# Kernel tuning notes

Hardware: AMD Instinct MI355X
Metric: run time of the kernel (lower is better)

The kernel has to match this reference:

```python
import jax, jax.numpy as jnp
import numpy as np

B, T, D, H, L, FF, V = 32, 64, 512, 8, 4, 2048, 128
HD = D // H
TEMP = 0.1
SCALE_BASE = 16.0
NEG = -1e9


def setup_inputs() -> dict:
    key = jax.random.key(0)
    cnt = [0]
    def nk():
        cnt[0] += 1
        return jax.random.fold_in(key, cnt[0])
    def rn(shape, s=0.02):
        return jax.random.normal(nk(), shape, dtype=jnp.float32) * s
    inp = {
        "target_tensor": jax.random.randint(nk(), (B, T), 0, V),
        "mol_encoding": jax.random.normal(nk(), (B, D), dtype=jnp.float32),
        "emb": rn((V, D), 1.0),
        "sa_in_w": rn((L, 3 * D, D)), "sa_in_b": jnp.zeros((L, 3 * D), jnp.float32),
        "sa_out_w": rn((L, D, D)), "sa_out_b": jnp.zeros((L, D), jnp.float32),
        "ca_in_w": rn((L, 3 * D, D)), "ca_in_b": jnp.zeros((L, 3 * D), jnp.float32),
        "ca_out_w": rn((L, D, D)), "ca_out_b": jnp.zeros((L, D), jnp.float32),
        "ff_w1": rn((L, FF, D)), "ff_b1": jnp.zeros((L, FF), jnp.float32),
        "ff_w2": rn((L, D, FF)), "ff_b2": jnp.zeros((L, D), jnp.float32),
        "n1_g": jnp.ones((L, D), jnp.float32), "n1_b": jnp.zeros((L, D), jnp.float32),
        "n2_g": jnp.ones((L, D), jnp.float32), "n2_b": jnp.zeros((L, D), jnp.float32),
        "n3_g": jnp.ones((L, D), jnp.float32), "n3_b": jnp.zeros((L, D), jnp.float32),
        "fn_g": jnp.ones((D,), jnp.float32), "fn_b": jnp.zeros((D,), jnp.float32),
        "out_w1": rn((2 * D, D)), "out_b1": jnp.zeros((2 * D,), jnp.float32),
        "out_w2": rn((1024, 2 * D)), "out_b2": jnp.zeros((1024,), jnp.float32),
        "out_w3": rn((V, 1024)), "out_b3": jnp.zeros((V,), jnp.float32),
    }
    return inp


def _ln(x, g, b, eps=1e-5):
    mu = x.mean(-1, keepdims=True)
    var = ((x - mu) ** 2).mean(-1, keepdims=True)
    return (x - mu) * jax.lax.rsqrt(var + eps) * g + b


def _xpos(x):
    # x: [B, T, D]; XPOS rotary with scale_base=16, downscale=False
    t, d = x.shape[1], x.shape[2]
    half = d // 2
    sv = (jnp.arange(0, d, 2, dtype=jnp.float32) + 0.4 * d) / (1.4 * d)      # [half]
    pos = jnp.arange(t, dtype=jnp.float32)
    scale = sv[None, :] ** (pos / SCALE_BASE)[:, None]                       # [t, half]
    inv_freq = 1.0 / (10000.0 ** (jnp.arange(half, dtype=jnp.float32) / half))
    ang = pos[:, None] * inv_freq[None, :]                                   # [t, half]
    sin = jnp.repeat(jnp.sin(ang) * scale, 2, axis=-1)                       # duplicate_interleave
    cos = jnp.repeat(jnp.cos(ang) * scale, 2, axis=-1)
    x1, x2 = x[..., ::2], x[..., 1::2]
    rot = jnp.stack((-x2, x1), axis=-1).reshape(x.shape)                     # rotate_every_two
    return x * cos + rot * sin


def _mha(q_in, k_in, v_in, in_w, in_b, out_w, out_b, mask):
    wq, wk, wv = jnp.split(in_w, 3, axis=0)
    bq, bk, bv = jnp.split(in_b, 3, axis=0)
    Bq, Tq = q_in.shape[0], q_in.shape[1]
    q = (q_in @ wq.T + bq).reshape(Bq, Tq, H, HD)
    k = (k_in @ wk.T + bk).reshape(Bq, -1, H, HD)
    v = (v_in @ wv.T + bv).reshape(Bq, -1, H, HD)
    scores = jnp.einsum('bqhd,bkhd->bhqk', q, k) / np.float32(np.sqrt(HD))
    if mask is not None:
        scores = jnp.where(mask, NEG, scores)
    p = jax.nn.softmax(scores, axis=-1)
    o = jnp.einsum('bhqk,bkhd->bqhd', p, v).reshape(Bq, Tq, D)
    return o @ out_w.T + out_b


def reference(target_tensor, mol_encoding, emb, sa_in_w, sa_in_b, sa_out_w, sa_out_b,
              ca_in_w, ca_in_b, ca_out_w, ca_out_b, ff_w1, ff_b1, ff_w2, ff_b2,
              n1_g, n1_b, n2_g, n2_b, n3_g, n3_b, fn_g, fn_b,
              out_w1, out_b1, out_w2, out_b2, out_w3, out_b3):
    memory = mol_encoding[:, None, :]                      # [B, 1, D]
    causal = jnp.triu(jnp.ones((T, T), bool), 1)
    samp_key = jax.random.key(1)

    def logits_at(pred, t):
        x = _xpos(emb[pred])                               # [B, T, D]
        mask = causal[None, None] | (pred == 0)[:, None, None, :]
        for i in range(L):
            a = _mha(x, x, x, sa_in_w[i], sa_in_b[i], sa_out_w[i], sa_out_b[i], mask)
            x = _ln(x + a, n1_g[i], n1_b[i])
            c = _mha(x, memory, memory, ca_in_w[i], ca_in_b[i], ca_out_w[i], ca_out_b[i], None)
            x = _ln(x + c, n2_g[i], n2_b[i])
            f = jax.nn.silu(x @ ff_w1[i].T + ff_b1[i]) @ ff_w2[i].T + ff_b2[i]
            x = _ln(x + f, n3_g[i], n3_b[i])
        x = _ln(x, fn_g, fn_b)
        h = jnp.take(x, t - 1, axis=1)                     # [B, D]
        h = jax.nn.gelu(h @ out_w1.T + out_b1, approximate=False)
        h = jax.nn.gelu(h @ out_w2.T + out_b2, approximate=False)
        return h @ out_w3.T + out_b3                       # [B, V]

    def step(pred, t):
        logits = logits_at(pred, t)
        lp = jax.nn.log_softmax(logits / TEMP, axis=-1)
        u = jax.random.uniform(jax.random.fold_in(samp_key, t), lp.shape)
        g = -jnp.log(-jnp.log(u + 1e-9) + 1e-9)
        tok = jnp.argmax(lp + g, axis=-1).astype(jnp.int32)
        return pred.at[:, t].set(tok), logits

    pred0 = jnp.zeros((B, T), jnp.int32).at[:, 0].set(1)
    pred, _ = jax.lax.scan(jax.checkpoint(step), pred0, jnp.arange(1, T))
    return pred
```

## Files before the change

### kernel.cpp

```cpp
#include <hip/hip_runtime.h>
#include <stdint.h>
#include <stddef.h>

#define BB 32
#define TT 64
#define DD 512
#define HH 8
#define HDIM 64
#define LL 4
#define FFD 2048
#define VV 128

#define NBLK 256
#define NTHR 512

__host__ __device__ inline uint32_t rotl32(uint32_t v, int n){ return (v << n) | (v >> (32 - n)); }

__host__ __device__ inline void tf2x32(uint32_t k0, uint32_t k1, uint32_t x0, uint32_t x1,
                                       uint32_t* o0, uint32_t* o1){
  uint32_t ks2 = k0 ^ k1 ^ 0x1BD11BDAu;
  x0 += k0; x1 += k1;
  x0 += x1; x1 = rotl32(x1,13); x1 ^= x0;
  x0 += x1; x1 = rotl32(x1,15); x1 ^= x0;
  x0 += x1; x1 = rotl32(x1,26); x1 ^= x0;
  x0 += x1; x1 = rotl32(x1, 6); x1 ^= x0;
  x0 += k1; x1 += ks2 + 1u;
  x0 += x1; x1 = rotl32(x1,17); x1 ^= x0;
  x0 += x1; x1 = rotl32(x1,29); x1 ^= x0;
  x0 += x1; x1 = rotl32(x1,16); x1 ^= x0;
  x0 += x1; x1 = rotl32(x1,24); x1 ^= x0;
  x0 += ks2; x1 += k0 + 2u;
  x0 += x1; x1 = rotl32(x1,13); x1 ^= x0;
  x0 += x1; x1 = rotl32(x1,15); x1 ^= x0;
  x0 += x1; x1 = rotl32(x1,26); x1 ^= x0;
  x0 += x1; x1 = rotl32(x1, 6); x1 ^= x0;
  x0 += k0; x1 += k1 + 3u;
  x0 += x1; x1 = rotl32(x1,17); x1 ^= x0;
  x0 += x1; x1 = rotl32(x1,29); x1 ^= x0;
  x0 += x1; x1 = rotl32(x1,16); x1 ^= x0;
  x0 += x1; x1 = rotl32(x1,24); x1 ^= x0;
  x0 += k1; x1 += ks2 + 4u;
  x0 += x1; x1 = rotl32(x1,13); x1 ^= x0;
  x0 += x1; x1 = rotl32(x1,15); x1 ^= x0;
  x0 += x1; x1 = rotl32(x1,26); x1 ^= x0;
  x0 += x1; x1 = rotl32(x1, 6); x1 ^= x0;
  x0 += ks2; x1 += k0 + 5u;
  *o0 = x0; *o1 = x1;
}

__device__ inline float dot_f4(const float* __restrict__ a, const float* __restrict__ w, int K){
  float acc = 0.f;
  const float4* a4 = (const float4*)a;
  const float4* w4 = (const float4*)w;
  int K4 = K >> 2;
  for (int k = 0; k < K4; ++k){
    float4 av = a4[k], wv = w4[k];
    acc = fmaf(av.x, wv.x, acc);
    acc = fmaf(av.y, wv.y, acc);
    acc = fmaf(av.z, wv.z, acc);
    acc = fmaf(av.w, wv.w, acc);
  }
  return acc;
}

__device__ inline float block_ln(float v, float g, float bb, float* red){
  __syncthreads();
  float s = v;
  #pragma unroll
  for (int off = 32; off; off >>= 1) s += __shfl_xor(s, off);
  if ((threadIdx.x & 63) == 0) red[threadIdx.x >> 6] = s;
  __syncthreads();
  float mu = (red[0]+red[1]+red[2]+red[3]+red[4]+red[5]+red[6]+red[7]) * (1.0f/512.0f);
  float dv = v - mu;
  float sq = dv * dv;
  #pragma unroll
  for (int off = 32; off; off >>= 1) sq += __shfl_xor(sq, off);
  __syncthreads();
  if ((threadIdx.x & 63) == 0) red[threadIdx.x >> 6] = sq;
  __syncthreads();
  float var = (red[0]+red[1]+red[2]+red[3]+red[4]+red[5]+red[6]+red[7]) * (1.0f/512.0f);
  return dv * (1.0f / sqrtf(var + 1e-5f)) * g + bb;
}

__device__ inline float row_reduce(float v, int wid, int j, float* wred){
  #pragma unroll
  for (int off = 32; off; off >>= 1) v += __shfl_xor(v, off);
  if ((threadIdx.x & 63) == 0) wred[wid] = v;
  __syncthreads();
  float r = wred[2*j] + wred[2*j+1];
  __syncthreads();
  return r;
}

__device__ __forceinline__ void gbar(unsigned* bar, int g){
  __syncthreads();
  if (threadIdx.x == 0){
    unsigned* cnt = bar + g*64;
    unsigned* gen = bar + g*64 + 16;
    __builtin_amdgcn_fence(__ATOMIC_RELEASE, "agent");
    unsigned old = __hip_atomic_load(gen, __ATOMIC_RELAXED, __HIP_MEMORY_SCOPE_AGENT);
    if (__hip_atomic_fetch_add(cnt, 1u, __ATOMIC_RELAXED, __HIP_MEMORY_SCOPE_AGENT) == 63u){
      __hip_atomic_store(cnt, 0u, __ATOMIC_RELAXED, __HIP_MEMORY_SCOPE_AGENT);
      __hip_atomic_fetch_add(gen, 1u, __ATOMIC_RELEASE, __HIP_MEMORY_SCOPE_AGENT);
    } else {
      while (__hip_atomic_load(gen, __ATOMIC_RELAXED, __HIP_MEMORY_SCOPE_AGENT) == old)
        __builtin_amdgcn_s_sleep(1);
    }
    __builtin_amdgcn_fence(__ATOMIC_ACQUIRE, "agent");
  }
  __syncthreads();
}

__global__ void k_tables(float* __restrict__ cosb, float* __restrict__ sinb){
  int tid = blockIdx.x * blockDim.x + threadIdx.x;
  int p = tid >> 8, i = tid & 255;
  float sv = (2.0f * (float)i + 204.8f) / 716.8f;
  float scale = powf(sv, (float)p / 16.0f);
  float invf = 1.0f / powf(10000.0f, (float)i / 256.0f);
  float ang = (float)p * invf;
  cosb[tid] = cosf(ang) * scale;
  sinb[tid] = sinf(ang) * scale;
}

__global__ void k_ca1(const float* __restrict__ mol, const float* __restrict__ w,
                      const float* __restrict__ bias, float* __restrict__ tmp){
  int tid = blockIdx.x * blockDim.x + threadIdx.x;
  int l = tid >> 14; int r = tid & 16383; int b = r >> 9; int d = r & 511;
  const float* wr = w + (size_t)l*3*DD*DD + (size_t)(2*DD + d)*DD;
  tmp[tid] = bias[l*3*DD + 2*DD + d] + dot_f4(mol + (size_t)b*DD, wr, DD);
}

__global__ void k_ca2(const float* __restrict__ tmp, const float* __restrict__ w,
                      const float* __restrict__ bias, float* __restrict__ cac){
  int tid = blockIdx.x * blockDim.x + threadIdx.x;
  int l = tid >> 14; int r = tid & 16383; int b = r >> 9; int d = r & 511;
  const float* wr = w + (size_t)l*DD*DD + (size_t)d*DD;
  cac[tid] = bias[l*DD + d] + dot_f4(tmp + ((size_t)l*BB + b)*DD, wr, DD);
}

__global__ void k_binit(unsigned* __restrict__ bar, int* __restrict__ pred){
  int tid = threadIdx.x;
  bar[tid] = 0u;
  pred[tid]        = ((tid & (TT-1)) == 0) ? 1 : 0;
  pred[tid + 1024] = (((tid + 1024) & (TT-1)) == 0) ? 1 : 0;
}

__global__ void k_pack32(const float* __restrict__ in, float* __restrict__ out,
                         int N, int K, int total){
  int tid = blockIdx.x * blockDim.x + threadIdx.x;
  if (tid >= total) return;
  int S = N * K;
  int l = tid / S, r = tid - l*S;
  int k32 = r / (32*N);
  int r2 = r - k32*32*N;
  int n = r2 >> 5, ku = r2 & 31;
  out[tid] = in[(size_t)l*S + (size_t)n*K + k32*32 + ku];
}

#define CELL8(WARR, KOFF)                                                     \
  _Pragma("unroll")                                                           \
  for (int q = 0; q < 8; ++q){                                                \
    float4 w = WARR[q];                                                       \
    const int kk = (KOFF) + q*4;                                              \
    _Pragma("unroll")                                                         \
    for (int r_ = 0; r_ < 8; ++r_){                                           \
      float4 x = *(const float4*)&sxp[r_*512 + kk];                           \
      a[r_]=fmaf(w.x,x.x,a[r_]); a[r_]=fmaf(w.y,x.y,a[r_]);                   \
      a[r_]=fmaf(w.z,x.z,a[r_]); a[r_]=fmaf(w.w,x.w,a[r_]);                   \
    }                                                                         \
  }

struct KParams {
  const float *emb, *sab, *sob, *f1b, *f2b;
  const float *g1,*b1,*g2,*b2,*g3,*b3,*fg,*fb;
  const float *o1b,*o2b,*o3w,*o3b;
  const float *cosb,*sinb,*cac;
  const float *sawP,*sowP,*f1wP,*f2wP,*o1wP,*o2wP;
  float *kc,*vc,*xl,*qb,*at,*ao,*x2,*fo,*h1,*xf,*hh1,*hh2,*ps3;
  int *pred;
  unsigned *bar;
};

__global__ __launch_bounds__(NTHR) void k_persist(KParams P){
  const int bid = blockIdx.x, tid = threadIdx.x;
  const int g = bid & 3;
  const int m = bid >> 2;
  const int wid = tid >> 6, lane = tid & 63;
  __shared__ __align__(16) float smem[17472];

  for (int t = 1; t < TT; ++t){
    const int pp = t - 1;

    for (int l = 0; l < LL; ++l){
      if (m < 24){
        float* sx   = smem;
        float* part = smem + 4096;
        float* srow = smem + 8192;
        if (l == 0){
          #pragma unroll
          for (int it = 0; it < 2; ++it){
            int j = it*4 + (tid >> 7), d4 = (tid & 127) * 4;
            int rb = g*8 + j;
            int tok = P.pred[rb*TT + pp];
            #pragma unroll
            for (int e = d4; e < d4 + 4; e += 2){
              int i = e >> 1;
              float c = P.cosb[pp*256 + i], s = P.sinb[pp*256 + i];
              float e0 = P.emb[(size_t)tok*DD + e];
              float e1 = P.emb[(size_t)tok*DD + e + 1];
              sx[j*512 + e]     = fmaf(e0, c, -(e1*s));
              sx[j*512 + e + 1] = fmaf(e1, c, e0*s);
            }
          }
        } else {
          if (tid < 8){
            float aa = 0.f, bq = 0.f;
            const float* pr = P.ps3 + (size_t)(g*8 + tid)*64;
            for (int s = 0; s < 32; ++s){ aa += pr[s*2]; bq += pr[s*2+1]; }
            float mu = aa * (1.0f/512.0f);
            float var = bq * (1.0f/512.0f) - mu*mu;
            srow[tid*2]   = mu;
            srow[tid*2+1] = 1.0f / sqrtf(var + 1e-5f);
          }
          __syncthreads();
          #pragma unroll
          for (int it = 0; it < 2; ++it){
            int j = it*4 + (tid >> 7), d4 = (tid & 127) * 4;
            int rb = g*8 + j;
            float mu = srow[j*2], rs = srow[j*2+1];
            float4 xv = *(const float4*)&P.x2[(size_t)rb*DD + d4];
            float4 fv = *(const float4*)&P.fo[(size_t)rb*DD + d4];
            const float* g3r = P.g3 + (size_t)(l-1)*DD;
            const float* b3r = P.b3 + (size_t)(l-1)*DD;
            float yv[4] = {xv.x+fv.x, xv.y+fv.y, xv.z+fv.z, xv.w+fv.w};
            #pragma unroll
            for (int i = 0; i < 4; ++i)
              sx[j*512 + d4 + i] = (yv[i]-mu)*rs*g3r[d4+i] + b3r[d4+i];
          }
        }
        __syncthreads();
        if (m == 0){
          #pragma unroll
          for (int it = 0; it < 2; ++it){
            int j = it*4 + (tid >> 7), d4 = (tid & 127) * 4;
            *(float4*)&P.xl[(size_t)(g*8+j)*DD + d4] = *(float4*)&sx[j*512 + d4];
          }
        }
        const int n0 = m*64;
        const float4* wb0 = (const float4*)P.sawP + ((size_t)l*16 + wid*2)*(1536*8)
                          + (size_t)(n0 + lane)*8;
        const float4* wb1 = wb0 + 1536*8;
        float4 w0[8], w1[8];
        #pragma unroll
        for (int q = 0; q < 8; ++q) w0[q] = wb0[q];
        #pragma unroll
        for (int q = 0; q < 8; ++q) w1[q] = wb1[q];
        float a[8] = {0.f,0.f,0.f,0.f,0.f,0.f,0.f,0.f};
        const float* sxp = sx;
        const int kb = wid*64;
        CELL8(w0, kb);
        CELL8(w1, kb + 32);
        #pragma unroll
        for (int r_ = 0; r_ < 8; ++r_) part[(wid*8 + r_)*64 + lane] = a[r_];
        __syncthreads();
        {
          int jr = tid >> 6, nl = tid & 63;
          int n = n0 + nl, rb2 = g*8 + jr;
          float s = P.sab[l*1536 + n];
          #pragma unroll
          for (int w = 0; w < 8; ++w) s += part[(w*8+jr)*64 + nl];
          if (n < DD){
            P.qb[(size_t)rb2*DD + n] = s;
          } else if (n < 2*DD){
            int h = (n - DD) >> 6, hd = (n - DD) & 63;
            P.kc[((((size_t)l*BB + rb2)*HH + h)*TT + pp)*HDIM + hd] = s;
          } else {
            int h = (n - 2*DD) >> 6, hd = (n - 2*DD) & 63;
            P.vc[((((size_t)l*BB + rb2)*HH + h)*TT + pp)*HDIM + hd] = s;
          }
        }
      }
      gbar(P.bar, g);

      {
        int bl = m >> 3, h = m & 7, rb = g*8 + bl;
        float* qs = smem; float* ps = smem + 64;
        if (tid < 64) qs[tid] = P.qb[(size_t)rb*DD + h*HDIM + tid];
        __syncthreads();
        if (tid < 64){
          const float* kb = P.kc + (((size_t)l*BB + rb)*HH + h)*TT*HDIM;
          float s = -INFINITY;
          if (lane <= pp && P.pred[rb*TT + lane] != 0){
            const float* kr = kb + lane*HDIM;
            float acc = 0.f;
            #pragma unroll
            for (int k2 = 0; k2 < HDIM; ++k2) acc = fmaf(qs[k2], kr[k2], acc);
            s = acc * 0.125f;
          }
          float mx = s;
          #pragma unroll
          for (int off = 32; off; off >>= 1) mx = fmaxf(mx, __shfl_xor(mx, off));
          float e = (s == -INFINITY) ? 0.f : expf(s - mx);
          float sum = e;
          #pragma unroll
          for (int off = 32; off; off >>= 1) sum += __shfl_xor(sum, off);
          ps[lane] = e / sum;
          const float* vb = P.vc + (((size_t)l*BB + rb)*HH + h)*TT*HDIM;
          float o = 0.f;
          int jj = 0;
          for (; jj + 8 <= t; jj += 8){
            float vv[8];
            #pragma unroll
            for (int u = 0; u < 8; ++u) vv[u] = vb[(jj+u)*HDIM + lane];
            #pragma unroll
            for (int u = 0; u < 8; ++u) o = fmaf(ps[jj+u], vv[u], o);
          }
          for (; jj <= pp; ++jj) o = fmaf(ps[jj], vb[jj*HDIM + lane], o);
          P.at[(size_t)rb*DD + h*HDIM + lane] = o;
        }
      }
      gbar(P.bar, g);

      if (m < 32){
        float* ats  = smem;
        float* part = smem + 4096;
        #pragma unroll
        for (int q = 0; q < 2; ++q){
          int fi = tid + q*512;
          int j = fi >> 7, c4 = fi & 127;
          *(float4*)&ats[j*512 + c4*4] = *(const float4*)&P.at[(size_t)(g*8+j)*DD + c4*4];
        }
        __syncthreads();
        const int n0 = m*16;
        const int jb = lane >> 4, nc = lane & 15;
        const float4* wb0 = (const float4*)P.sowP + ((size_t)l*16 + wid*2)*(512*8)
                          + (size_t)(n0 + nc)*8;
        const float4* wb1 = wb0 + 512*8;
        float4 w0[8], w1[8];
        #pragma unroll
        for (int q = 0; q < 8; ++q) w0[q] = wb0[q];
        #pragma unroll
        for (int q = 0; q < 8; ++q) w1[q] = wb1[q];
        float ac0 = 0.f, ac1 = 0.f;
        const int kb = wid*64;
        #pragma unroll
        for (int q = 0; q < 8; ++q){
          float4 w = w0[q];
          float4 xa = *(const float4*)&ats[jb*512 + kb + q*4];
          float4 xb = *(const float4*)&ats[(jb+4)*512 + kb + q*4];
          ac0=fmaf(w.x,xa.x,ac0); ac0=fmaf(w.y,xa.y,ac0); ac0=fmaf(w.z,xa.z,ac0); ac0=fmaf(w.w,xa.w,ac0);
          ac1=fmaf(w.x,xb.x,ac1); ac1=fmaf(w.y,xb.y,ac1); ac1=fmaf(w.z,xb.z,ac1); ac1=fmaf(w.w,xb.w,ac1);
        }
        #pragma unroll
        for (int q = 0; q < 8; ++q){
          float4 w = w1[q];
          float4 xa = *(const float4*)&ats[jb*512 + kb + 32 + q*4];
          float4 xb = *(const float4*)&ats[(jb+4)*512 + kb + 32 + q*4];
          ac0=fmaf(w.x,xa.x,ac0); ac0=fmaf(w.y,xa.y,ac0); ac0=fmaf(w.z,xa.z,ac0); ac0=fmaf(w.w,xa.w,ac0);
          ac1=fmaf(w.x,xb.x,ac1); ac1=fmaf(w.y,xb.y,ac1); ac1=fmaf(w.z,xb.z,ac1); ac1=fmaf(w.w,xb.w,ac1);
        }
        part[wid*128 + jb*16 + nc]       = ac0;
        part[wid*128 + (jb+4)*16 + nc]   = ac1;
        __syncthreads();
        if (tid < 128){
          int jb2 = tid >> 4, nc2 = tid & 15, n = n0 + nc2;
          float s = P.sob[l*DD + n];
          #pragma unroll
          for (int w = 0; w < 8; ++w) s += part[w*128 + jb2*16 + nc2];
          P.ao[(size_t)(g*8+jb2)*DD + n] = s;
        }
      }
      gbar(P.bar, g);

      if (m < 32){
        float* sx2  = smem;
        float* part = smem + 4096;
        float* wred = smem + 8192;
        #pragma unroll
        for (int it = 0; it < 2; ++it){
          int j = tid >> 7, d4 = (tid & 127) * 4;
          int jr = it*4 + j;
          int rb = g*8 + jr;
          float4 xlv = *(const float4*)&P.xl[(size_t)rb*DD + d4];
          float4 aov = *(const float4*)&P.ao[(size_t)rb*DD + d4];
          float y[4] = {xlv.x+aov.x, xlv.y+aov.y, xlv.z+aov.z, xlv.w+aov.w};
          float s = ((y[0]+y[1])+y[2])+y[3];
          float mu = row_reduce(s, wid, j, wred) * (1.0f/512.0f);
          float dv[4], sq = 0.f;
          #pragma unroll
          for (int i = 0; i < 4; ++i){ dv[i] = y[i]-mu; sq += dv[i]*dv[i]; }
          float rs = 1.0f / sqrtf(row_reduce(sq, wid, j, wred) * (1.0f/512.0f) + 1e-5f);
          float z[4];
          #pragma unroll
          for (int i = 0; i < 4; ++i){
            int d = d4 + i;
            z[i] = dv[i]*rs*P.g1[l*DD+d] + P.b1[l*DD+d] + P.cac[((size_t)l*BB + rb)*DD + d];
          }
          float s2 = ((z[0]+z[1])+z[2])+z[3];
          float mu2 = row_reduce(s2, wid, j, wred) * (1.0f/512.0f);
          float dz[4], sq2 = 0.f;
          #pragma unroll
          for (int i = 0; i < 4; ++i){ dz[i] = z[i]-mu2; sq2 += dz[i]*dz[i]; }
          float rs2 = 1.0f / sqrtf(row_reduce(sq2, wid, j, wred) * (1.0f/512.0f) + 1e-5f);
          #pragma unroll
          for (int i = 0; i < 4; ++i){
            int d = d4 + i;
            float x2v = dz[i]*rs2*P.g2[l*DD+d] + P.b2[l*DD+d];
            sx2[jr*512 + d] = x2v;
          }
        }
        __syncthreads();
        if (m == 0){
          #pragma unroll
          for (int it = 0; it < 2; ++it){
            int jr = it*4 + (tid >> 7), d4 = (tid & 127) * 4;
            *(float4*)&P.x2[(size_t)(g*8+jr)*DD + d4] = *(float4*)&sx2[jr*512 + d4];
          }
        }
        const int n0 = m*64;
        const float4* wb0 = (const float4*)P.f1wP + ((size_t)l*16 + wid*2)*(2048*8)
                          + (size_t)(n0 + lane)*8;
        const float4* wb1 = wb0 + 2048*8;
        float4 w0[8], w1[8];
        #pragma unroll
        for (int q = 0; q < 8; ++q) w0[q] = wb0[q];
        #pragma unroll
        for (int q = 0; q < 8; ++q) w1[q] = wb1[q];
        float a[8] = {0.f,0.f,0.f,0.f,0.f,0.f,0.f,0.f};
        const float* sxp = sx2;
        const int kb = wid*64;
        CELL8(w0, kb);
        CELL8(w1, kb + 32);
        #pragma unroll
        for (int r_ = 0; r_ < 8; ++r_) part[(wid*8 + r_)*64 + lane] = a[r_];
        __syncthreads();
        {
          int jr = tid >> 6, nl = tid & 63;
          int n = n0 + nl;
          float v = P.f1b[l*FFD + n];
          #pragma unroll
          for (int w = 0; w < 8; ++w) v += part[(w*8+jr)*64 + nl];
          P.h1[(size_t)(g*8+jr)*FFD + n] = v / (1.0f + expf(-v));
        }
      }
      gbar(P.bar, g);

      if (m < 32){
        float* sh1  = smem;
        float* part = smem + 16384;
        #pragma unroll
        for (int q = 0; q < 8; ++q){
          int fi = tid + q*512;
          int j = fi >> 9, c4 = fi & 511;
          *(float4*)&sh1[j*2048 + c4*4] = *(const float4*)&P.h1[(size_t)(g*8+j)*FFD + c4*4];
        }
        __syncthreads();
        const int n0 = m*16;
        const int jb = lane >> 4, nc = lane & 15;
        const float4* base = (const float4*)P.f2wP + ((size_t)l*64 + wid*8)*(512*8)
                           + (size_t)(n0 + nc)*8;
        float ac0 = 0.f, ac1 = 0.f;
        #pragma unroll
        for (int cc = 0; cc < 4; ++cc){
          const float4* b0 = base + (size_t)(cc*2)*(512*8);
          const float4* b1 = b0 + 512*8;
          float4 w0[8], w1[8];
          #pragma unroll
          for (int q = 0; q < 8; ++q) w0[q] = b0[q];
          #pragma unroll
          for (int q = 0; q < 8; ++q) w1[q] = b1[q];
          const int kb = wid*256 + cc*64;
          #pragma unroll
          for (int q = 0; q < 8; ++q){
            float4 w = w0[q];
            float4 xa = *(const float4*)&sh1[jb*2048 + kb + q*4];
            float4 xb = *(const float4*)&sh1[(jb+4)*2048 + kb + q*4];
            ac0=fmaf(w.x,xa.x,ac0); ac0=fmaf(w.y,xa.y,ac0); ac0=fmaf(w.z,xa.z,ac0); ac0=fmaf(w.w,xa.w,ac0);
            ac1=fmaf(w.x,xb.x,ac1); ac1=fmaf(w.y,xb.y,ac1); ac1=fmaf(w.z,xb.z,ac1); ac1=fmaf(w.w,xb.w,ac1);
          }
          #pragma unroll
          for (int q = 0; q < 8; ++q){
            float4 w = w1[q];
            float4 xa = *(const float4*)&sh1[jb*2048 + kb + 32 + q*4];
            float4 xb = *(const float4*)&sh1[(jb+4)*2048 + kb + 32 + q*4];
            ac0=fmaf(w.x,xa.x,ac0); ac0=fmaf(w.y,xa.y,ac0); ac0=fmaf(w.z,xa.z,ac0); ac0=fmaf(w.w,xa.w,ac0);
            ac1=fmaf(w.x,xb.x,ac1); ac1=fmaf(w.y,xb.y,ac1); ac1=fmaf(w.z,xb.z,ac1); ac1=fmaf(w.w,xb.w,ac1);
          }
        }
        part[wid*128 + jb*16 + nc]     = ac0;
        part[wid*128 + (jb+4)*16 + nc] = ac1;
        __syncthreads();
        if (tid < 128){
          int jb2 = tid >> 4, nc2 = tid & 15, n = n0 + nc2;
          int rb2 = g*8 + jb2;
          float val = P.f2b[l*DD + n];
          #pragma unroll
          for (int w = 0; w < 8; ++w) val += part[w*128 + jb2*16 + nc2];
          P.fo[(size_t)rb2*DD + n] = val;
          float y = P.x2[(size_t)rb2*DD + n] + val;
          float s1 = y, sq = y*y;
          #pragma unroll
          for (int off = 1; off < 16; off <<= 1){
            s1 += __shfl_xor(s1, off);
            sq += __shfl_xor(sq, off);
          }
          if (nc2 == 0){
            P.ps3[(size_t)(rb2*32 + m)*2]     = s1;
            P.ps3[(size_t)(rb2*32 + m)*2 + 1] = sq;
          }
        }
      }
      gbar(P.bar, g);
    }

    if (m < 8){
      int rb = g*8 + m, d = tid;
      float y = P.x2[(size_t)rb*DD + d] + P.fo[(size_t)rb*DD + d];
      float xv = block_ln(y, P.g3[3*DD + d], P.b3[3*DD + d], smem);
      float o  = block_ln(xv, P.fg[d], P.fb[d], smem);
      P.xf[(size_t)rb*DD + d] = o;
    }
    gbar(P.bar, g);

    if (m < 32){
      float* sxf  = smem;
      float* part = smem + 4096;
      #pragma unroll
      for (int q = 0; q < 2; ++q){
        int fi = tid + q*512;
        int j = fi >> 7, c4 = fi & 127;
        *(float4*)&sxf[j*512 + c4*4] = *(const float4*)&P.xf[(size_t)(g*8+j)*DD + c4*4];
      }
      __syncthreads();
      const int n0 = m*32;
      const int jh = lane >> 5, nc = lane & 31;
      const float4* wb0 = (const float4*)P.o1wP + (size_t)(wid*2)*(1024*8)
                        + (size_t)(n0 + nc)*8;
      const float4* wb1 = wb0 + 1024*8;
      float4 w0[8], w1[8];
      #pragma unroll
      for (int q = 0; q < 8; ++q) w0[q] = wb0[q];
      #pragma unroll
      for (int q = 0; q < 8; ++q) w1[q] = wb1[q];
      float ac[4] = {0.f,0.f,0.f,0.f};
      const int kb = wid*64;
      #pragma unroll
      for (int q = 0; q < 8; ++q){
        float4 w = w0[q];
        #pragma unroll
        for (int ai = 0; ai < 4; ++ai){
          float4 x = *(const float4*)&sxf[(jh+2*ai)*512 + kb + q*4];
          ac[ai]=fmaf(w.x,x.x,ac[ai]); ac[ai]=fmaf(w.y,x.y,ac[ai]);
          ac[ai]=fmaf(w.z,x.z,ac[ai]); ac[ai]=fmaf(w.w,x.w,ac[ai]);
        }
      }
      #pragma unroll
      for (int q = 0; q < 8; ++q){
        float4 w = w1[q];
        #pragma unroll
        for (int ai = 0; ai < 4; ++ai){
          float4 x = *(const float4*)&sxf[(jh+2*ai)*512 + kb + 32 + q*4];
          ac[ai]=fmaf(w.x,x.x,ac[ai]); ac[ai]=fmaf(w.y,x.y,ac[ai]);
          ac[ai]=fmaf(w.z,x.z,ac[ai]); ac[ai]=fmaf(w.w,x.w,ac[ai]);
        }
      }
      #pragma unroll
      for (int ai = 0; ai < 4; ++ai) part[(wid*8 + (jh+2*ai))*32 + nc] = ac[ai];
      __syncthreads();
      if (tid < 256){
        int row = tid >> 5, nc2 = tid & 31, n = n0 + nc2;
        float aa = P.o1b[n];
        #pragma unroll
        for (int w = 0; w < 8; ++w) aa += part[(w*8+row)*32 + nc2];
        P.hh1[(size_t)(g*8+row)*1024 + n] = 0.5f * aa * (1.0f + erff(aa / 1.41421356237309504880f));
      }
    }
    gbar(P.bar, g);

    if (m < 32){
      float* sh   = smem;
      float* part = smem + 8192;
      #pragma unroll
      for (int q = 0; q < 4; ++q){
        int fi = tid + q*512;
        int j = fi >> 8, c4 = fi & 255;
        *(float4*)&sh[j*1024 + c4*4] = *(const float4*)&P.hh1[(size_t)(g*8+j)*1024 + c4*4];
      }
      __syncthreads();
      const int n0 = m*32;
      const int jh = lane >> 5, nc = lane & 31;
      const float4* base = (const float4*)P.o2wP + (size_t)(wid*4)*(1024*8)
                         + (size_t)(n0 + nc)*8;
      float ac[4] = {0.f,0.f,0.f,0.f};
      #pragma unroll
      for (int cc = 0; cc < 2; ++cc){
        const float4* b0 = base + (size_t)(cc*2)*(1024*8);
        const float4* b1 = b0 + 1024*8;
        float4 w0[8], w1[8];
        #pragma unroll
        for (int q = 0; q < 8; ++q) w0[q] = b0[q];
        #pragma unroll
        for (int q = 0; q < 8; ++q) w1[q] = b1[q];
        const int kb = wid*128 + cc*64;
        #pragma unroll
        for (int q = 0; q < 8; ++q){
          float4 w = w0[q];
          #pragma unroll
          for (int ai = 0; ai < 4; ++ai){
            float4 x = *(const float4*)&sh[(jh+2*ai)*1024 + kb + q*4];
            ac[ai]=fmaf(w.x,x.x,ac[ai]); ac[ai]=fmaf(w.y,x.y,ac[ai]);
            ac[ai]=fmaf(w.z,x.z,ac[ai]); ac[ai]=fmaf(w.w,x.w,ac[ai]);
          }
        }
        #pragma unroll
        for (int q = 0; q < 8; ++q){
          float4 w = w1[q];
          #pragma unroll
          for (int ai = 0; ai < 4; ++ai){
            float4 x = *(const float4*)&sh[(jh+2*ai)*1024 + kb + 32 + q*4];
            ac[ai]=fmaf(w.x,x.x,ac[ai]); ac[ai]=fmaf(w.y,x.y,ac[ai]);
            ac[ai]=fmaf(w.z,x.z,ac[ai]); ac[ai]=fmaf(w.w,x.w,ac[ai]);
          }
        }
      }
      #pragma unroll
      for (int ai = 0; ai < 4; ++ai) part[(wid*8 + (jh+2*ai))*32 + nc] = ac[ai];
      __syncthreads();
      if (tid < 256){
        int row = tid >> 5, nc2 = tid & 31, n = n0 + nc2;
        float aa = P.o2b[n];
        #pragma unroll
        for (int w = 0; w < 8; ++w) aa += part[(w*8+row)*32 + nc2];
        P.hh2[(size_t)(g*8+row)*1024 + n] = 0.5f * aa * (1.0f + erff(aa / 1.41421356237309504880f));
      }
    }
    gbar(P.bar, g);

    if (m < 8){
      int rb = g*8 + m, v = tid;
      float* hrow = smem;
      float* red  = smem + 1024;
      int*   redi = (int*)(smem + 1032);
      for (int k = tid; k < 1024; k += NTHR) hrow[k] = P.hh2[(size_t)rb*1024 + k];
      __syncthreads();
      float sv = 0.f;
      if (tid < 128){
        float acc = P.o3b[v] + dot_f4(hrow, P.o3w + (size_t)v*1024, 1024);
        sv = acc / 0.1f;
      }
      float mx = (tid < 128) ? sv : -INFINITY;
      #pragma unroll
      for (int off = 32; off; off >>= 1) mx = fmaxf(mx, __shfl_xor(mx, off));
      __syncthreads();
      if (tid < 128 && (tid & 63) == 0) red[tid >> 6] = mx;
      __syncthreads();
      mx = fmaxf(red[0], red[1]);
      float e = (tid < 128) ? expf(sv - mx) : 0.f;
      float sum = e;
      #pragma unroll
      for (int off = 32; off; off >>= 1) sum += __shfl_xor(sum, off);
      __syncthreads();
      if (tid < 128 && (tid & 63) == 0) red[tid >> 6] = sum;
      __syncthreads();
      sum = red[0] + red[1];
      float bv = -INFINITY; int bi = 0x7fffffff;
      if (tid < 128){
        float lp = (sv - mx) - logf(sum);
        uint32_t kk0, kk1, o0, o1;
        tf2x32(0u, 1u, 0u, (uint32_t)t, &kk0, &kk1);
        tf2x32(kk0, kk1, 0u, (uint32_t)(rb*VV + v), &o0, &o1);
        uint32_t bits = o0 ^ o1;
        float u = __uint_as_float((bits >> 9) | 0x3F800000u) - 1.0f;
        float gg = -logf(-logf(u + 1e-9f) + 1e-9f);
        bv = lp + gg; bi = v;
      }
      #pragma unroll
      for (int off = 32; off; off >>= 1){
        float ov = __shfl_xor(bv, off);
        int   oi = __shfl_xor(bi, off);
        if (ov > bv || (ov == bv && oi < bi)){ bv = ov; bi = oi; }
      }
      __syncthreads();
      if (tid < 128 && (tid & 63) == 0){ red[tid >> 6] = bv; redi[tid >> 6] = bi; }
      __syncthreads();
      if (tid == 0){
        float v0 = red[0], v1 = red[1]; int i0 = redi[0], i1 = redi[1];
        P.pred[rb*TT + t] = (v1 > v0 || (v1 == v0 && i1 < i0)) ? i1 : i0;
      }
    }
    gbar(P.bar, g);
  }
}

extern "C" void kernel_launch(void* const* d_in, const int* in_sizes, int n_in,
                              void* d_out, int out_size, void* d_ws, size_t ws_size,
                              hipStream_t stream){
  (void)in_sizes; (void)n_in; (void)out_size; (void)ws_size;
  const float* mol      = (const float*)d_in[1];
  const float* sa_in_w  = (const float*)d_in[3];
  const float* sa_out_w = (const float*)d_in[5];
  const float* ca_in_w  = (const float*)d_in[7];
  const float* ca_in_b  = (const float*)d_in[8];
  const float* ca_out_w = (const float*)d_in[9];
  const float* ca_out_b = (const float*)d_in[10];
  const float* ff_w1    = (const float*)d_in[11];
  const float* ff_w2    = (const float*)d_in[13];
  const float* out_w1   = (const float*)d_in[23];
  const float* out_w2   = (const float*)d_in[25];

  KParams P;
  P.emb = (const float*)d_in[2];
  P.sab = (const float*)d_in[4];
  P.sob = (const float*)d_in[6];
  P.f1b = (const float*)d_in[12];
  P.f2b = (const float*)d_in[14];
  P.g1  = (const float*)d_in[15];
  P.b1  = (const float*)d_in[16];
  P.g2  = (const float*)d_in[17];
  P.b2  = (const float*)d_in[18];
  P.g3  = (const float*)d_in[19];
  P.b3  = (const float*)d_in[20];
  P.fg  = (const float*)d_in[21];
  P.fb  = (const float*)d_in[22];
  P.o1b = (const float*)d_in[24];
  P.o2b = (const float*)d_in[26];
  P.o3w = (const float*)d_in[27];
  P.o3b = (const float*)d_in[28];

  unsigned* bar = (unsigned*)d_ws;
  float* ws = (float*)d_ws + 1024;
  float* cosb   = ws;
  float* sinb   = cosb + 16384;
  float* ca_tmp = sinb + 16384;
  float* cac    = ca_tmp + 65536;
  float* kc     = cac + 65536;
  float* vc     = kc + 4194304;
  float* xl     = vc + 4194304;
  float* qb     = xl + 16384;
  float* at     = qb + 16384;
  float* ao     = at + 16384;
  float* x2     = ao + 16384;
  float* fo     = x2 + 16384;
  float* h1     = fo + 16384;
  float* xf     = h1 + 65536;
  float* hh1    = xf + 16384;
  float* hh2    = hh1 + 32768;
  float* ps3    = hh2 + 32768;
  float* sawP   = ps3 + 2048;
  float* sowP   = sawP + 3145728;
  float* f1wP   = sowP + 1048576;
  float* f2wP   = f1wP + 4194304;
  float* o1wP   = f2wP + 4194304;
  float* o2wP   = o1wP + 524288;

  P.cosb = cosb; P.sinb = sinb; P.cac = cac;
  P.kc = kc; P.vc = vc; P.xl = xl; P.qb = qb; P.at = at; P.ao = ao;
  P.x2 = x2; P.fo = fo; P.h1 = h1; P.xf = xf; P.hh1 = hh1; P.hh2 = hh2;
  P.ps3 = ps3;
  P.sawP = sawP; P.sowP = sowP; P.f1wP = f1wP; P.f2wP = f2wP;
  P.o1wP = o1wP; P.o2wP = o2wP;
  P.pred = (int*)d_out;
  P.bar = bar;

  k_binit<<<1, 1024, 0, stream>>>(bar, P.pred);
  k_tables<<<64, 256, 0, stream>>>(cosb, sinb);
  k_ca1<<<256, 256, 0, stream>>>(mol, ca_in_w, ca_in_b, ca_tmp);
  k_ca2<<<256, 256, 0, stream>>>(ca_tmp, ca_out_w, ca_out_b, cac);

  {
    int t1 = 4*1536*512;  k_pack32<<<(t1+255)/256, 256, 0, stream>>>(sa_in_w,  sawP, 1536, 512,  t1);
    int t2 = 4*512*512;   k_pack32<<<(t2+255)/256, 256, 0, stream>>>(sa_out_w, sowP,  512, 512,  t2);
    int t3 = 4*2048*512;  k_pack32<<<(t3+255)/256, 256, 0, stream>>>(ff_w1,    f1wP, 2048, 512,  t3);
    int t4 = 4*512*2048;  k_pack32<<<(t4+255)/256, 256, 0, stream>>>(ff_w2,    f2wP,  512, 2048, t4);
    int t5 = 1024*512;    k_pack32<<<(t5+255)/256, 256, 0, stream>>>(out_w1,   o1wP, 1024, 512,  t5);
    int t6 = 1024*1024;   k_pack32<<<(t6+255)/256, 256, 0, stream>>>(out_w2,   o2wP, 1024, 1024, t6);
  }

  k_persist<<<NBLK, NTHR, 0, stream>>>(P);
}
```

Before: 26.35 ms.

## Replace flat grid-group barrier with hierarchical epoch-based counter tree

Each of the four 64-block groups used one shared atomic counter plus a generation word for its barrier. The new barrier uses monotonically increasing epochs and a two-level tree: 8-block sub-counters feed a per-half counter, and the two halves exchange flags. The last arriver of each half publishes a generation value that all blocks in that half poll. The aim is to reduce atomic contention on a single counter and to drop the reset store. The cost is more atomic hops on the critical path and a larger barrier workspace, which shifts the workspace offset.

```diff
diff --git a/kernel.cpp b/kernel.cpp
--- a/kernel.cpp
+++ b/kernel.cpp
@@ -92,20 +92,31 @@
   return r;
 }
 
-__device__ __forceinline__ void gbar(unsigned* bar, int g){
+__device__ __forceinline__ void gbar(unsigned* bar, int g, int m, unsigned epoch){
   __syncthreads();
   if (threadIdx.x == 0){
-    unsigned* cnt = bar + g*64;
-    unsigned* gen = bar + g*64 + 16;
     __builtin_amdgcn_fence(__ATOMIC_RELEASE, "agent");
-    unsigned old = __hip_atomic_load(gen, __ATOMIC_RELAXED, __HIP_MEMORY_SCOPE_AGENT);
-    if (__hip_atomic_fetch_add(cnt, 1u, __ATOMIC_RELAXED, __HIP_MEMORY_SCOPE_AGENT) == 63u){
-      __hip_atomic_store(cnt, 0u, __ATOMIC_RELAXED, __HIP_MEMORY_SCOPE_AGENT);
-      __hip_atomic_fetch_add(gen, 1u, __ATOMIC_RELEASE, __HIP_MEMORY_SCOPE_AGENT);
-    } else {
-      while (__hip_atomic_load(gen, __ATOMIC_RELAXED, __HIP_MEMORY_SCOPE_AGENT) == old)
-        __builtin_amdgcn_s_sleep(1);
+    const int h   = m & 1;
+    const int k   = m >> 1;
+    const int sub = k >> 3;
+    const int gh  = g*2 + h;
+    unsigned* subcnt  = bar + gh*64 + sub*16;
+    unsigned* halfcnt = bar + 1024 + gh*16;
+    unsigned* hflag   = bar + 1280 + gh*16;
+    unsigned* peer    = bar + 1280 + (g*2 + (1-h))*16;
+    unsigned* hgen    = bar + 1536 + gh*16;
+    unsigned old = __hip_atomic_fetch_add(subcnt, 1u, __ATOMIC_RELAXED, __HIP_MEMORY_SCOPE_AGENT);
+    if (old == 8u*epoch - 1u){
+      unsigned o2 = __hip_atomic_fetch_add(halfcnt, 1u, __ATOMIC_RELAXED, __HIP_MEMORY_SCOPE_AGENT);
+      if (o2 == 4u*epoch - 1u){
+        __hip_atomic_store(hflag, epoch, __ATOMIC_RELAXED, __HIP_MEMORY_SCOPE_AGENT);
+        while (__hip_atomic_load(peer, __ATOMIC_RELAXED, __HIP_MEMORY_SCOPE_AGENT) < epoch)
+          __builtin_amdgcn_s_sleep(1);
+        __hip_atomic_store(hgen, epoch, __ATOMIC_RELAXED, __HIP_MEMORY_SCOPE_AGENT);
+      }
     }
+    while (__hip_atomic_load(hgen, __ATOMIC_RELAXED, __HIP_MEMORY_SCOPE_AGENT) < epoch)
+      __builtin_amdgcn_s_sleep(1);
     __builtin_amdgcn_fence(__ATOMIC_ACQUIRE, "agent");
   }
   __syncthreads();
@@ -141,6 +152,7 @@
 __global__ void k_binit(unsigned* __restrict__ bar, int* __restrict__ pred){
   int tid = threadIdx.x;
   bar[tid] = 0u;
+  bar[tid + 1024] = 0u;
   pred[tid]        = ((tid & (TT-1)) == 0) ? 1 : 0;
   pred[tid + 1024] = (((tid + 1024) & (TT-1)) == 0) ? 1 : 0;
 }
@@ -187,6 +199,7 @@
   const int m = bid >> 2;
   const int wid = tid >> 6, lane = tid & 63;
   __shared__ __align__(16) float smem[17472];
+  unsigned epoch = 0;
 
   for (int t = 1; t < TT; ++t){
     const int pp = t - 1;
@@ -280,7 +293,7 @@
           }
         }
       }
-      gbar(P.bar, g);
+      gbar(P.bar, g, m, ++epoch);
 
       {
         int bl = m >> 3, h = m & 7, rb = g*8 + bl;
@@ -319,7 +332,7 @@
           P.at[(size_t)rb*DD + h*HDIM + lane] = o;
         }
       }
-      gbar(P.bar, g);
+      gbar(P.bar, g, m, ++epoch);
 
       if (m < 32){
         float* ats  = smem;
@@ -370,7 +383,7 @@
           P.ao[(size_t)(g*8+jb2)*DD + n] = s;
         }
       }
-      gbar(P.bar, g);
+      gbar(P.bar, g, m, ++epoch);
 
       if (m < 32){
         float* sx2  = smem;
@@ -443,7 +456,7 @@
           P.h1[(size_t)(g*8+jr)*FFD + n] = v / (1.0f + expf(-v));
         }
       }
-      gbar(P.bar, g);
+      gbar(P.bar, g, m, ++epoch);
 
       if (m < 32){
         float* sh1  = smem;
@@ -510,7 +523,7 @@
           }
         }
       }
-      gbar(P.bar, g);
+      gbar(P.bar, g, m, ++epoch);
     }
 
     if (m < 8){
@@ -520,7 +533,7 @@
       float o  = block_ln(xv, P.fg[d], P.fb[d], smem);
       P.xf[(size_t)rb*DD + d] = o;
     }
-    gbar(P.bar, g);
+    gbar(P.bar, g, m, ++epoch);
 
     if (m < 32){
       float* sxf  = smem;
@@ -575,7 +588,7 @@
         P.hh1[(size_t)(g*8+row)*1024 + n] = 0.5f * aa * (1.0f + erff(aa / 1.41421356237309504880f));
       }
     }
-    gbar(P.bar, g);
+    gbar(P.bar, g, m, ++epoch);
 
     if (m < 32){
       float* sh   = smem;
@@ -634,7 +647,7 @@
         P.hh2[(size_t)(g*8+row)*1024 + n] = 0.5f * aa * (1.0f + erff(aa / 1.41421356237309504880f));
       }
     }
-    gbar(P.bar, g);
+    gbar(P.bar, g, m, ++epoch);
 
     if (m < 8){
       int rb = g*8 + m, v = tid;
@@ -688,7 +701,7 @@
         P.pred[rb*TT + t] = (v1 > v0 || (v1 == v0 && i1 < i0)) ? i1 : i0;
       }
     }
-    gbar(P.bar, g);
+    gbar(P.bar, g, m, ++epoch);
   }
 }
 
@@ -728,7 +741,7 @@
   P.o3b = (const float*)d_in[28];
 
   unsigned* bar = (unsigned*)d_ws;
-  float* ws = (float*)d_ws + 1024;
+  float* ws = (float*)d_ws + 2048;
   float* cosb   = ws;
   float* sinb   = cosb + 16384;
   float* ca_tmp = sinb + 16384;
```

Result: faster. 24.77 ms (-6.0%).
